# Performance work log

Measured on AMD Instinct MI355X. Metric: run time of the kernel, lower is better.

## Reference

```python
import jax, jax.numpy as jnp
from jax import lax
import numpy as np

NH = 4                      # num_heads in CrossScaleCom
KS = [3, 5, 7, 9]           # per-head depthwise kernel sizes
WS = 2                      # window_size in LocalFeatureGuided
GGM_K = 7                   # guide-token generator kernel size


def _dwconv(x, w, stride, pad):
    # depthwise conv: w has shape (C, 1, k, k), feature_group_count = C
    return lax.conv_general_dilated(
        x, w, (stride, stride), [(pad, pad), (pad, pad)],
        feature_group_count=x.shape[1],
        dimension_numbers=("NCHW", "OIHW", "NCHW"))


def _forward(x, dw_w0, dw_b0, dw_w1, dw_b1, dw_w2, dw_b2, dw_w3, dw_b3,
             csc_w, csc_b, bn_gamma, bn_beta, bn_mean, bn_var,
             ggm_w, ggm_b, qkv_w, qkv_b, proj_w, proj_b):
    B, C, H, W = x.shape
    cph = C // NH
    # ---- CrossScaleCom: per-head multi-scale depthwise convs ----
    xh = x.reshape(B, NH, cph, H, W)
    dws = [(dw_w0, dw_b0), (dw_w1, dw_b1), (dw_w2, dw_b2), (dw_w3, dw_b3)]
    heads = [_dwconv(xh[:, i], w, 1, KS[i] // 2) + b[None, :, None, None]
             for i, (w, b) in enumerate(dws)]
    y = jnp.stack(heads, 1)                      # (B, NH, cph, H, W)
    y = y.transpose(0, 2, 1, 3, 4).reshape(B, C, H, W)  # channel shuffle
    y = jnp.einsum("bchw,oc->bohw", y, csc_w) + csc_b[None, :, None, None]
    Co = y.shape[1]
    # ---- LocalFeatureGuided ----
    # ggm: BatchNorm (eval) -> GELU (exact) -> depthwise conv k=7 stride=WS
    inv = bn_gamma / jnp.sqrt(bn_var + 1e-5)
    g = (y - bn_mean[None, :, None, None]) * inv[None, :, None, None] \
        + bn_beta[None, :, None, None]
    g = jax.nn.gelu(g, approximate=False)
    g = _dwconv(g, ggm_w, WS, GGM_K // 2) + ggm_b[None, :, None, None]  # (B,Co,Ho,Wo)
    Ho, Wo = H // WS, W // WS
    L = Ho * Wo
    # unfold(kernel=WS, stride=WS) -> (B, Co, WS*WS, L), torch unfold ordering
    xu = y.reshape(B, Co, Ho, WS, Wo, WS).transpose(0, 1, 3, 5, 2, 4)
    xu = xu.reshape(B, Co, WS * WS, L)
    tokens = jnp.concatenate([g.reshape(B, Co, 1, L), xu], axis=2)  # (B,Co,5,L)
    # 1x1 conv over channel dim == einsum
    qkv = jnp.einsum("bcpl,oc->bopl", tokens, qkv_w) + qkv_b[None, :, None, None]
    q, k, v = jnp.split(qkv, 3, axis=1)          # each (B, Co, 5, L)
    # tiny 5x5 attention per (batch, channel), contracting over windows L
    attn = jnp.einsum("bcpl,bcql->bcpq", q, k) / (Co ** 0.5)
    attn = jax.nn.softmax(attn, axis=-1)
    out = jnp.einsum("bcpq,bcql->bcpl", attn, v)  # (B, Co, 5, L)
    out = out[:, :, 0, :].reshape(B, Co, Ho, Wo)  # guide-token output
    out = jnp.einsum("bchw,oc->bohw", out, proj_w) + proj_b[None, :, None, None]
    return out


def setup_inputs() -> dict:
    key = jax.random.key(0)
    ks = jax.random.split(key, 16)
    B, Cin, Cout, H, W = 8, 64, 128, 224, 224
    cph = Cin // NH
    s = 0.05
    d = {"x": jax.random.normal(ks[0], (B, Cin, H, W), jnp.float32)}
    for i, kk in enumerate(KS):
        d[f"dw_w{i}"] = jax.random.normal(ks[1 + i], (cph, 1, kk, kk), jnp.float32) * s
        d[f"dw_b{i}"] = jnp.zeros((cph,), jnp.float32)
    d["csc_w"] = jax.random.normal(ks[5], (Cout, Cin), jnp.float32) * s
    d["csc_b"] = jnp.zeros((Cout,), jnp.float32)
    d["bn_gamma"] = jnp.ones((Cout,), jnp.float32)
    d["bn_beta"] = jnp.zeros((Cout,), jnp.float32)
    d["bn_mean"] = jnp.zeros((Cout,), jnp.float32)
    d["bn_var"] = jnp.ones((Cout,), jnp.float32)
    d["ggm_w"] = jax.random.normal(ks[6], (Cout, 1, GGM_K, GGM_K), jnp.float32) * s
    d["ggm_b"] = jnp.zeros((Cout,), jnp.float32)
    d["qkv_w"] = jax.random.normal(ks[7], (3 * Cout, Cout), jnp.float32) * s
    d["qkv_b"] = jnp.zeros((3 * Cout,), jnp.float32)
    d["proj_w"] = jax.random.normal(ks[8], (Cout, Cout), jnp.float32) * s
    d["proj_b"] = jnp.zeros((Cout,), jnp.float32)
    return d


def reference(x, dw_w0, dw_b0, dw_w1, dw_b1, dw_w2, dw_b2, dw_w3, dw_b3,
              csc_w, csc_b, bn_gamma, bn_beta, bn_mean, bn_var,
              ggm_w, ggm_b, qkv_w, qkv_b, proj_w, proj_b):
    return _forward(x, dw_w0, dw_b0, dw_w1, dw_b1, dw_w2, dw_b2, dw_w3, dw_b3,
                    csc_w, csc_b, bn_gamma, bn_beta, bn_mean, bn_var,
                    ggm_w, ggm_b, qkv_w, qkv_b, proj_w, proj_b)
```

## Files before the change

kernel.cpp:

```cpp
#include <hip/hip_runtime.h>

#define BB 8
#define CIN 64
#define CO 128
#define Hdim 224
#define Wdim 224
#define HWt (224*224)
#define HO 112
#define WO 112
#define Lt (112*112)

typedef unsigned short u16;
typedef short bf16x8 __attribute__((ext_vector_type(8)));
typedef float f32x4  __attribute__((ext_vector_type(4)));
#define MFMA16(a,b,c) __builtin_amdgcn_mfma_f32_16x16x32_bf16((a),(b),(c),0,0,0)

__device__ inline u16 f2bf(float f) {
    union { float f; unsigned u; } v; v.f = f;
    unsigned r = (v.u + 0x7fffu + ((v.u >> 16) & 1u)) >> 16;
    return (u16)r;
}
__device__ inline float bf2f(u16 h) {
    union { unsigned u; float f; } v; v.u = ((unsigned)h) << 16; return v.f;
}
__device__ inline float uasf(unsigned u) {
    union { unsigned u; float f; } v; v.u = u; return v.f;
}

__device__ inline float gelu_fast(float x) {
    float z  = x * 0.7071067811865476f;
    float az = fabsf(z);
    float t  = __builtin_amdgcn_rcpf(fmaf(0.3275911f, az, 1.0f));
    float p  = fmaf(fmaf(fmaf(fmaf(1.061405429f, t, -1.453152027f), t,
                    1.421413741f), t, -0.284496736f), t, 0.254829592f);
    float e  = __expf(-z * z);
    float er = copysignf(1.0f - p * t * e, z);
    return 0.5f * x * (1.0f + er);
}

template<int HEAD>
__global__ __launch_bounds__(256) void dw_conv(
    const float* __restrict__ x, const float* __restrict__ w,
    const float* __restrict__ bias, u16* __restrict__ dwb)
{
    constexpr int K   = 3 + 2*HEAD;
    constexpr int PAD = HEAD + 1;
    constexpr int R   = 32 + 2*PAD;
    const int tile = blockIdx.x;
    const int c    = blockIdx.y;
    const int b    = blockIdx.z;
    const int th = (tile/7)*32, tw = (tile%7)*32;
    __shared__ float patch[R*40];
    const int tid = threadIdx.x;
    const float* xin = x + (size_t)(b*CIN + HEAD*16 + c)*HWt;
    for (int idx = tid; idx < R*40; idx += 256) {
        int r = idx / 40, cc = idx - r*40;
        int gy = th - PAD + r, gx = tw - 4 + cc;
        float v = 0.f;
        if (gy >= 0 && gy < Hdim && gx >= 0 && gx < Wdim) v = xin[gy*Wdim + gx];
        patch[idx] = v;
    }
    float wreg[K*K];
    const float* wp = w + c*K*K;
    #pragma unroll
    for (int i = 0; i < K*K; i++) wreg[i] = wp[i];
    const float bv = bias[c];
    __syncthreads();

    const int ty = tid >> 3, x0 = (tid & 7) * 4;
    float acc[4] = {bv, bv, bv, bv};
    #pragma unroll
    for (int ky = 0; ky < K; ky++) {
        float rr[12];
        *(float4*)&rr[0] = *(const float4*)&patch[(ty+ky)*40 + x0];
        *(float4*)&rr[4] = *(const float4*)&patch[(ty+ky)*40 + x0 + 4];
        *(float4*)&rr[8] = *(const float4*)&patch[(ty+ky)*40 + x0 + 8];
        #pragma unroll
        for (int kx = 0; kx < K; kx++) {
            const float wv = wreg[ky*K + kx];
            #pragma unroll
            for (int j = 0; j < 4; j++)
                acc[j] = fmaf(rr[j + kx + 4 - PAD], wv, acc[j]);
        }
    }
    const int s = c*4 + HEAD;
    u16 o4[4] = {f2bf(acc[0]), f2bf(acc[1]), f2bf(acc[2]), f2bf(acc[3])};
    *(uint2*)&dwb[(size_t)(b*CIN + s)*HWt + (th+ty)*Wdim + tw + x0] = *(uint2*)o4;
}

__global__ __launch_bounds__(256) void csc_mfma(
    const float* __restrict__ W, const float* __restrict__ bias,
    const u16* __restrict__ dwb, u16* __restrict__ y4)
{
    const int b  = blockIdx.z;
    const int p0 = blockIdx.x * 128;
    __shared__ u16 Abuf[128*72];
    __shared__ u16 Tbuf[32*132];
    const int tid = threadIdx.x;
    const int wv = tid >> 6, ln = tid & 63;
    const int mh = (wv >> 1)*64, nh = (wv & 1)*64;
    const int lm = ln & 15, kq = ln >> 4;
    for (int t = tid; t < 1024; t += 256) {
        int r = t >> 3, kk = (t & 7)*8;
        const float* src = &W[r*64 + kk];
        float4 f0 = *(const float4*)src, f1 = *(const float4*)(src+4);
        u16 tmp[8] = {f2bf(f0.x),f2bf(f0.y),f2bf(f0.z),f2bf(f0.w),
                      f2bf(f1.x),f2bf(f1.y),f2bf(f1.z),f2bf(f1.w)};
        *(uint4*)&Abuf[r*72 + kk] = *(uint4*)tmp;
    }
    const u16* Db = dwb + (size_t)b*CIN*HWt;
    f32x4 acc[4][4];
    #pragma unroll
    for (int i=0;i<4;i++)
        #pragma unroll
        for (int j=0;j<4;j++) acc[i][j] = (f32x4){0.f,0.f,0.f,0.f};

    for (int kc = 0; kc < 64; kc += 32) {
        __syncthreads();
        for (int t = tid; t < 512; t += 256) {
            int k = t >> 4, n0 = (t & 15)*8;
            *(uint4*)&Tbuf[k*132 + n0] = *(const uint4*)&Db[(size_t)(kc+k)*HWt + p0 + n0];
        }
        __syncthreads();
        bf16x8 af[4], bfr[4];
        #pragma unroll
        for (int tm=0;tm<4;tm++)
            af[tm] = *(bf16x8*)&Abuf[(mh + tm*16 + lm)*72 + kc + kq*8];
        #pragma unroll
        for (int tn=0;tn<4;tn++) {
            int n = nh + tn*16 + lm;
            #pragma unroll
            for (int j=0;j<8;j++) bfr[tn][j] = (short)Tbuf[(kq*8+j)*132 + n];
        }
        #pragma unroll
        for (int tm=0;tm<4;tm++)
            #pragma unroll
            for (int tn=0;tn<4;tn++)
                acc[tm][tn] = MFMA16(af[tm], bfr[tn], acc[tm][tn]);
    }
    #pragma unroll
    for (int tm=0;tm<4;tm++) {
        #pragma unroll
        for (int r=0;r<4;r++) {
            int o = mh + tm*16 + kq*4 + r;
            float bb = bias[o];
            #pragma unroll
            for (int tn=0;tn<4;tn++) {
                int p = p0 + nh + tn*16 + lm;
                int gy = p / 224, gx = p - gy*224;
                int w = (gy&1)*2 + (gx&1);
                y4[((size_t)(b*CO + o)*4 + w)*Lt + (gy>>1)*WO + (gx>>1)]
                    = f2bf(acc[tm][tn][r] + bb);
            }
        }
    }
}

__global__ __launch_bounds__(512) void ggm_kernel(const u16* __restrict__ y4,
    const float* __restrict__ gamma, const float* __restrict__ beta,
    const float* __restrict__ mean, const float* __restrict__ var,
    const float* __restrict__ gw, const float* __restrict__ gb,
    u16* __restrict__ gbf)
{
    const int ho0 = blockIdx.x * 16;
    const int c   = blockIdx.y;
    const int b   = blockIdx.z;
    __shared__ float patch[37*240];
    const int tid = threadIdx.x;

    const float inv = gamma[c] * rsqrtf(var[c] + 1e-5f);
    const float bsh = fmaf(-mean[c], inv, beta[c]);
    const u16* ybc = y4 + (size_t)(b*CO + c)*4*Lt;

    float wk[49];
    const float* wp = gw + c*49;
    #pragma unroll
    for (int i = 0; i < 49; i++) wk[i] = wp[i];
    const float bv = gb[c];

    for (int idx = tid; idx < 37*60; idx += 512) {
        int r = idx / 60, j = idx - r*60;
        int gy = 2*ho0 - 3 + r;
        float4 v = make_float4(0.f, 0.f, 0.f, 0.f);
        if (gy >= 0 && gy < Hdim && j >= 2 && j <= 57) {
            const u16* pe = ybc + (size_t)((gy&1)*2)*Lt + (gy>>1)*WO + (2*j - 4);
            unsigned e = *(const unsigned*)pe;
            unsigned o = *(const unsigned*)(pe + Lt);
            v.x = gelu_fast(fmaf(uasf(e << 16),         inv, bsh));
            v.y = gelu_fast(fmaf(uasf(o << 16),         inv, bsh));
            v.z = gelu_fast(fmaf(uasf(e & 0xffff0000u), inv, bsh));
            v.w = gelu_fast(fmaf(uasf(o & 0xffff0000u), inv, bsh));
        }
        *(float4*)&patch[idx*4] = v;
    }
    __syncthreads();

    if (tid < 448) {
        const int n = tid % 56;
        const int g = tid / 56;
        float acc[2][2] = {{bv, bv}, {bv, bv}};
        #pragma unroll
        for (int rr = 0; rr < 9; rr++) {
            const float* row = &patch[(4*g + rr)*240 + 4*n + 4];
            float f[12];
            *(float4*)&f[0] = *(const float4*)&row[0];
            *(float4*)&f[4] = *(const float4*)&row[4];
            *(float4*)&f[8] = *(const float4*)&row[8];
            #pragma unroll
            for (int i = 0; i < 2; i++) {
                const int ky = rr - 2*i;
                if (ky >= 0 && ky <= 6) {
                    #pragma unroll
                    for (int kx = 0; kx < 7; kx++) {
                        const float wv = wk[ky*7 + kx];
                        acc[i][0] = fmaf(f[kx + 1], wv, acc[i][0]);
                        acc[i][1] = fmaf(f[kx + 3], wv, acc[i][1]);
                    }
                }
            }
        }
        u16* gout = gbf + (size_t)(b*CO + c)*Lt;
        #pragma unroll
        for (int i = 0; i < 2; i++) {
            u16 o2[2] = {f2bf(acc[i][0]), f2bf(acc[i][1])};
            *(unsigned*)&gout[(ho0 + 2*g + i)*WO + 2*n] = *(unsigned*)o2;
        }
    }
}

__global__ __launch_bounds__(256) void G_mfma(
    const u16* __restrict__ gbf, const u16* __restrict__ y4,
    float* __restrict__ Gpart, float* __restrict__ Spart)
{
    const int b = blockIdx.z, p = blockIdx.y, split = blockIdx.x;
    const u16* Ab = gbf + (size_t)b*CO*Lt;
    const u16* Bb; int brs;
    if (p == 0) { Bb = Ab; brs = Lt; }
    else        { Bb = y4 + ((size_t)b*CO*4 + (p-1))*Lt; brs = 4*Lt; }
    __shared__ u16 Abuf[128*72];
    __shared__ u16 Bbuf[128*72];
    const int tid = threadIdx.x;
    const int wv = tid >> 6, ln = tid & 63;
    const int mh = (wv >> 1)*64, nh = (wv & 1)*64;
    const int lm = ln & 15, kq = ln >> 4;
    f32x4 acc[4][4];
    #pragma unroll
    for (int i=0;i<4;i++)
        #pragma unroll
        for (int j=0;j<4;j++) acc[i][j] = (f32x4){0.f,0.f,0.f,0.f};
    bf16x8 af_s;
    #pragma unroll
    for (int j=0;j<8;j++) af_s[j] = (lm == 0) ? (short)0x3F80 : (short)0;
    f32x4 acc_s[4];
    #pragma unroll
    for (int j=0;j<4;j++) acc_s[j] = (f32x4){0.f,0.f,0.f,0.f};
    const bool sWave = (mh == 0);

    for (int ci = split; ci < 196; ci += 16) {
        const int l0 = ci*64;
        __syncthreads();
        for (int t = tid; t < 1024; t += 256) {
            int r = t >> 3, kk = (t & 7)*8;
            *(uint4*)&Abuf[r*72 + kk] = *(const uint4*)&Ab[(size_t)r*Lt  + l0 + kk];
            *(uint4*)&Bbuf[r*72 + kk] = *(const uint4*)&Bb[(size_t)r*brs + l0 + kk];
        }
        __syncthreads();
        #pragma unroll
        for (int ks = 0; ks < 2; ks++) {
            bf16x8 af[4], bfr[4];
            #pragma unroll
            for (int tm=0;tm<4;tm++)
                af[tm]  = *(bf16x8*)&Abuf[(mh + tm*16 + lm)*72 + ks*32 + kq*8];
            #pragma unroll
            for (int tn=0;tn<4;tn++)
                bfr[tn] = *(bf16x8*)&Bbuf[(nh + tn*16 + lm)*72 + ks*32 + kq*8];
            #pragma unroll
            for (int tm=0;tm<4;tm++)
                #pragma unroll
                for (int tn=0;tn<4;tn++)
                    acc[tm][tn] = MFMA16(af[tm], bfr[tn], acc[tm][tn]);
            if (sWave) {
                #pragma unroll
                for (int tn=0;tn<4;tn++)
                    acc_s[tn] = MFMA16(af_s, bfr[tn], acc_s[tn]);
            }
        }
    }
    float* Go = Gpart + ((size_t)(split*40) + b*5 + p)*CO*CO;
    #pragma unroll
    for (int tm=0;tm<4;tm++)
        #pragma unroll
        for (int r=0;r<4;r++) {
            int mrow = mh + tm*16 + kq*4 + r;
            #pragma unroll
            for (int tn=0;tn<4;tn++)
                Go[mrow*CO + nh + tn*16 + lm] = acc[tm][tn][r];
        }
    if (sWave && kq == 0) {
        float* So = Spart + ((size_t)(split*40) + b*5 + p)*CO;
        #pragma unroll
        for (int tn=0;tn<4;tn++)
            So[nh + tn*16 + lm] = acc_s[tn][0];
    }
}

__global__ void G_reduce(const float* __restrict__ Gpart,
                         const float* __restrict__ Spart,
                         float* __restrict__ G, float* __restrict__ S)
{
    const int bp = blockIdx.x;
    const int i4 = (blockIdx.y*256 + threadIdx.x)*4;
    float4 s = make_float4(0.f, 0.f, 0.f, 0.f);
    #pragma unroll
    for (int sp = 0; sp < 16; sp++) {
        float4 v = *(const float4*)&Gpart[((size_t)(sp*40) + bp)*CO*CO + i4];
        s.x += v.x; s.y += v.y; s.z += v.z; s.w += v.w;
    }
    *(float4*)&G[(size_t)bp*CO*CO + i4] = s;
    if (blockIdx.y == 0 && threadIdx.x < CO) {
        float ss = 0.f;
        #pragma unroll
        for (int sp = 0; sp < 16; sp++)
            ss += Spart[((size_t)(sp*40) + bp)*CO + threadIdx.x];
        S[(size_t)bp*CO + threadIdx.x] = ss;
    }
}

__global__ __launch_bounds__(256) void fused_logits_kernel(
    const float* __restrict__ G, const float* __restrict__ S,
    const float* __restrict__ qkv_w, const float* __restrict__ qkv_b,
    float* __restrict__ lg)
{
    const int p = blockIdx.x, b = blockIdx.y;
    __shared__ float Wl[32*132];
    __shared__ float Al[32*132];
    __shared__ float KGl[128*128];
    const int tid = threadIdx.x;
    const int og = (tid >> 4) * 8;
    const int pg = (tid & 15) * 8;
    const float* Gp = G + (size_t)(b*5 + p)*CO*CO;
    float acc[8][8];
    #pragma unroll
    for (int i=0;i<8;i++)
        #pragma unroll
        for (int j=0;j<8;j++) acc[i][j]=0.f;

    for (int kc = 0; kc < 128; kc += 32) {
        __syncthreads();
        for (int t = tid; t < 4096; t += 256) {
            int kk = t & 31, o = t >> 5;
            Wl[kk*132 + o] = Gp[(size_t)o*CO + kc + kk];
            Al[kk*132 + o] = qkv_w[(size_t)(CO + o)*CO + kc + kk];
        }
        __syncthreads();
        #pragma unroll 4
        for (int kk = 0; kk < 32; kk++) {
            float wv[8], av[8];
            *(float4*)&wv[0] = *(const float4*)&Wl[kk*132+og];
            *(float4*)&wv[4] = *(const float4*)&Wl[kk*132+og+4];
            *(float4*)&av[0] = *(const float4*)&Al[kk*132+pg];
            *(float4*)&av[4] = *(const float4*)&Al[kk*132+pg+4];
            #pragma unroll
            for (int i=0;i<8;i++)
                #pragma unroll
                for (int j=0;j<8;j++)
                    acc[i][j] = fmaf(wv[i], av[j], acc[i][j]);
        }
    }
    #pragma unroll
    for (int i=0;i<8;i++) {
        #pragma unroll
        for (int j=0;j<8;j+=4)
            *(float4*)&KGl[(og+i)*128 + pg + j] = *(float4*)&acc[i][j];
    }
    __syncthreads();
    if (tid < 128) {
        const int c = tid;
        const float qb = qkv_b[c], kb = qkv_b[CO + c];
        const float* S0 = S + (size_t)b*5*CO;
        const float* Sp = S0 + p*CO;
        const float* qwrow = qkv_w + (size_t)c*CO;
        const float* kwrow = qkv_w + (size_t)(CO + c)*CO;
        float sq = qb * 12544.f, ks = 0.f, s = 0.f;
        for (int c2 = 0; c2 < CO; c2++) {
            sq = fmaf(qwrow[c2], S0[c2], sq);
            ks = fmaf(kwrow[c2], Sp[c2], ks);
            s  = fmaf(qwrow[c2], KGl[c2*128 + c], s);
        }
        lg[(size_t)(b*5 + p)*CO + c] = s + qb*ks + kb*sq;
    }
}

__global__ void softmax5_kernel(const float* __restrict__ lg, float* __restrict__ a)
{
    const int b = blockIdx.x, c = threadIdx.x;
    float v[5];
    #pragma unroll
    for (int p=0;p<5;p++) v[p] = lg[(size_t)(b*5 + p)*CO + c];
    const float scl = 0.08838834764831845f;
    float mx = v[0];
    #pragma unroll
    for (int p=1;p<5;p++) mx = fmaxf(mx, v[p]);
    float e[5], sum = 0.f;
    #pragma unroll
    for (int p=0;p<5;p++){ e[p] = __expf((v[p]-mx)*scl); sum += e[p]; }
    const float rs = 1.f/sum;
    #pragma unroll
    for (int p=0;p<5;p++) a[((size_t)b*CO + c)*5 + p] = e[p]*rs;
}

__global__ void F_kernel(const float* __restrict__ proj_w,
    const float* __restrict__ qkv_w, const float* __restrict__ a,
    u16* __restrict__ Fb)
{
    const int b = blockIdx.z, p = blockIdx.y;
    const int o  = blockIdx.x*2 + (threadIdx.x>>7);
    const int cp = threadIdx.x & 127;
    const float* vw = qkv_w + 2*CO*CO;
    float s = 0.f;
    for (int c=0;c<CO;c++)
        s = fmaf(proj_w[o*CO+c] * a[((size_t)b*CO+c)*5 + p], vw[c*CO+cp], s);
    Fb[(((size_t)(b*5+p))*CO + o)*CO + cp] = f2bf(s);
}

__global__ void bias_kernel(const float* __restrict__ proj_w,
    const float* __restrict__ proj_b, const float* __restrict__ qkv_b,
    float* __restrict__ biasout)
{
    const int o = threadIdx.x;
    const float* vb = qkv_b + 2*CO;
    float s = proj_b[o];
    for (int c=0;c<CO;c++) s = fmaf(proj_w[o*CO+c], vb[c], s);
    biasout[o] = s;
}

__global__ __launch_bounds__(256) void final_mfma(
    const u16* __restrict__ Fb, const u16* __restrict__ gbf,
    const u16* __restrict__ y4, const float* __restrict__ biasout,
    float* __restrict__ out)
{
    const int b = blockIdx.z;
    const int p0 = blockIdx.x * 128;
    __shared__ u16 Abuf[128*40];
    __shared__ u16 Tbuf[32*132];
    const int tid = threadIdx.x;
    const int wv = tid >> 6, ln = tid & 63;
    const int mh = (wv >> 1)*64, nh = (wv & 1)*64;
    const int lm = ln & 15, kq = ln >> 4;
    f32x4 acc[4][4];
    #pragma unroll
    for (int i=0;i<4;i++)
        #pragma unroll
        for (int j=0;j<4;j++) acc[i][j] = (f32x4){0.f,0.f,0.f,0.f};

    for (int ph = 0; ph < 5; ph++) {
        const u16* Fp = Fb + (size_t)(b*5 + ph)*CO*CO;
        const u16* Bb; int brs;
        if (ph == 0) { Bb = gbf + (size_t)b*CO*Lt; brs = Lt; }
        else         { Bb = y4 + ((size_t)b*CO*4 + (ph-1))*Lt; brs = 4*Lt; }
        for (int kc = 0; kc < CO; kc += 32) {
            __syncthreads();
            for (int t = tid; t < 512; t += 256) {
                int r = t >> 2, kk = (t & 3)*8;
                *(uint4*)&Abuf[r*40 + kk] = *(const uint4*)&Fp[r*CO + kc + kk];
            }
            for (int t = tid; t < 512; t += 256) {
                int k = t >> 4, n0 = (t & 15)*8;
                *(uint4*)&Tbuf[k*132 + n0] = *(const uint4*)&Bb[(size_t)(kc+k)*brs + p0 + n0];
            }
            __syncthreads();
            bf16x8 af[4], bfr[4];
            #pragma unroll
            for (int tm=0;tm<4;tm++)
                af[tm] = *(bf16x8*)&Abuf[(mh + tm*16 + lm)*40 + kq*8];
            #pragma unroll
            for (int tn=0;tn<4;tn++) {
                int n = nh + tn*16 + lm;
                #pragma unroll
                for (int j=0;j<8;j++) bfr[tn][j] = (short)Tbuf[(kq*8+j)*132 + n];
            }
            #pragma unroll
            for (int tm=0;tm<4;tm++)
                #pragma unroll
                for (int tn=0;tn<4;tn++)
                    acc[tm][tn] = MFMA16(af[tm], bfr[tn], acc[tm][tn]);
        }
    }
    float* Ob = out + (size_t)b*CO*Lt;
    #pragma unroll
    for (int tm=0;tm<4;tm++) {
        #pragma unroll
        for (int r=0;r<4;r++) {
            int o = mh + tm*16 + kq*4 + r;
            float bb = biasout[o];
            #pragma unroll
            for (int tn=0;tn<4;tn++)
                Ob[(size_t)o*Lt + p0 + nh + tn*16 + lm] = acc[tm][tn][r] + bb;
        }
    }
}

extern "C" void kernel_launch(void* const* d_in, const int* in_sizes, int n_in,
                              void* d_out, int out_size, void* d_ws, size_t ws_size,
                              hipStream_t stream) {
    const float* x      = (const float*)d_in[0];
    const float* dw_w0  = (const float*)d_in[1];
    const float* dw_b0  = (const float*)d_in[2];
    const float* dw_w1  = (const float*)d_in[3];
    const float* dw_b1  = (const float*)d_in[4];
    const float* dw_w2  = (const float*)d_in[5];
    const float* dw_b2  = (const float*)d_in[6];
    const float* dw_w3  = (const float*)d_in[7];
    const float* dw_b3  = (const float*)d_in[8];
    const float* csc_w  = (const float*)d_in[9];
    const float* csc_b  = (const float*)d_in[10];
    const float* bn_g   = (const float*)d_in[11];
    const float* bn_b   = (const float*)d_in[12];
    const float* bn_m   = (const float*)d_in[13];
    const float* bn_v   = (const float*)d_in[14];
    const float* ggm_w  = (const float*)d_in[15];
    const float* ggm_b  = (const float*)d_in[16];
    const float* qkv_w  = (const float*)d_in[17];
    const float* qkv_b  = (const float*)d_in[18];
    const float* proj_w = (const float*)d_in[19];
    const float* proj_b = (const float*)d_in[20];
    float* out = (float*)d_out;

    char* ws = (char*)d_ws;
    u16*   y4  = (u16*)(ws);
    u16*   dwb = (u16*)(ws + 102760448);
    u16*   gbf = (u16*)(ws + 154140672);
    float* G   = (float*)(ws + 179830784);
    float* lgb = (float*)(ws + 182452224);
    u16*   Fb  = (u16*)  (ws + 182472704);
    float* S   = (float*)(ws + 183783424);
    float* aw  = (float*)(ws + 183803904);
    float* bo  = (float*)(ws + 183824384);
    float* Gpart = (float*)(ws + 102760448);
    float* Spart = (float*)(ws + 144703488);

    dw_conv<0><<<dim3(49, 16, 8), 256, 0, stream>>>(x, dw_w0, dw_b0, dwb);
    dw_conv<1><<<dim3(49, 16, 8), 256, 0, stream>>>(x, dw_w1, dw_b1, dwb);
    dw_conv<2><<<dim3(49, 16, 8), 256, 0, stream>>>(x, dw_w2, dw_b2, dwb);
    dw_conv<3><<<dim3(49, 16, 8), 256, 0, stream>>>(x, dw_w3, dw_b3, dwb);

    csc_mfma<<<dim3(392, 1, 8), 256, 0, stream>>>(csc_w, csc_b, dwb, y4);

    ggm_kernel<<<dim3(7, 128, 8), 512, 0, stream>>>(
        y4, bn_g, bn_b, bn_m, bn_v, ggm_w, ggm_b, gbf);

    G_mfma<<<dim3(16, 5, 8), 256, 0, stream>>>(gbf, y4, Gpart, Spart);
    G_reduce<<<dim3(40, 16), 256, 0, stream>>>(Gpart, Spart, G, S);

    fused_logits_kernel<<<dim3(5, 8), 256, 0, stream>>>(G, S, qkv_w, qkv_b, lgb);

    softmax5_kernel<<<dim3(8), 128, 0, stream>>>(lgb, aw);

    F_kernel<<<dim3(64, 5, 8), 256, 0, stream>>>(proj_w, qkv_w, aw, Fb);
    bias_kernel<<<dim3(1), 128, 0, stream>>>(proj_w, proj_b, qkv_b, bo);

    final_mfma<<<dim3(98, 1, 8), 256, 0, stream>>>(Fb, gbf, y4, bo, out);
}
```

Before: 617.7 us.

## Tile csc GEMM in 2D spatially for paired stores; widen G split when workspace allows

The csc_mfma kernel now tiles pixels as 4 rows by 32 columns and permutes the columns inside shared memory. Each lane then holds two horizontally adjacent pixels of the same unfold window and writes them as one 32-bit store into y4, where before it issued scattered 16-bit stores. Separately, G_mfma raises its split-K count from 16 to 32 when the workspace is large enough, giving more blocks for the 40 (batch, token) GEMMs at the cost of more partial sums for G_reduce to add. Shared-memory staging becomes scalar scattered 16-bit writes, which may add bank conflicts.

```diff
diff --git a/kernel.cpp b/kernel.cpp
--- a/kernel.cpp
+++ b/kernel.cpp
@@ -92,8 +92,9 @@
     const float* __restrict__ W, const float* __restrict__ bias,
     const u16* __restrict__ dwb, u16* __restrict__ y4)
 {
-    const int b  = blockIdx.z;
-    const int p0 = blockIdx.x * 128;
+    const int b   = blockIdx.z;
+    const int gy0 = (blockIdx.x / 7) * 4;
+    const int gx0 = (blockIdx.x % 7) * 32;
     __shared__ u16 Abuf[128*72];
     __shared__ u16 Tbuf[32*132];
     const int tid = threadIdx.x;
@@ -118,8 +119,20 @@
     for (int kc = 0; kc < 64; kc += 32) {
         __syncthreads();
         for (int t = tid; t < 512; t += 256) {
-            int k = t >> 4, n0 = (t & 15)*8;
-            *(uint4*)&Tbuf[k*132 + n0] = *(const uint4*)&Db[(size_t)(kc+k)*HWt + p0 + n0];
+            int k = t >> 4, s = t & 15;
+            int ry = s >> 2, seg = s & 3;
+            uint4 v = *(const uint4*)&Db[(size_t)(kc+k)*HWt
+                                         + (gy0+ry)*224 + gx0 + seg*8];
+            unsigned uu[4] = {v.x, v.y, v.z, v.w};
+            #pragma unroll
+            for (int u = 0; u < 8; u++) {
+                int gxo = seg*8 + u;
+                int lmd = ((gxo >> 2) << 1) | (gxo & 1);
+                int tnd = ((gxo >> 1) & 1) | ((ry & 1) << 1);
+                int nhd = (ry >> 1) << 6;
+                u16 val = (u16)((uu[u >> 1] >> ((u & 1)*16)) & 0xffff);
+                Tbuf[k*132 + nhd + tnd*16 + lmd] = val;
+            }
         }
         __syncthreads();
         bf16x8 af[4], bfr[4];
@@ -138,19 +151,22 @@
             for (int tn=0;tn<4;tn++)
                 acc[tm][tn] = MFMA16(af[tm], bfr[tn], acc[tm][tn]);
     }
+    const int gyh = (gy0 >> 1) + (nh >> 6);
+    const int gxh = (gx0 >> 1) + 2*(lm >> 1);
     #pragma unroll
     for (int tm=0;tm<4;tm++) {
         #pragma unroll
         for (int r=0;r<4;r++) {
             int o = mh + tm*16 + kq*4 + r;
             float bb = bias[o];
-            #pragma unroll
-            for (int tn=0;tn<4;tn++) {
-                int p = p0 + nh + tn*16 + lm;
-                int gy = p / 224, gx = p - gy*224;
-                int w = (gy&1)*2 + (gx&1);
-                y4[((size_t)(b*CO + o)*4 + w)*Lt + (gy>>1)*WO + (gx>>1)]
-                    = f2bf(acc[tm][tn][r] + bb);
+            size_t obase = (size_t)(b*CO + o)*4*Lt;
+            #pragma unroll
+            for (int pr=0;pr<2;pr++) {
+                int w = (pr << 1) | (lm & 1);
+                u16 p2[2] = {f2bf(acc[tm][2*pr][r] + bb),
+                             f2bf(acc[tm][2*pr+1][r] + bb)};
+                *(unsigned*)&y4[obase + (size_t)w*Lt + gyh*WO + gxh]
+                    = *(unsigned*)p2;
             }
         }
     }
@@ -230,7 +246,7 @@
 
 __global__ __launch_bounds__(256) void G_mfma(
     const u16* __restrict__ gbf, const u16* __restrict__ y4,
-    float* __restrict__ Gpart, float* __restrict__ Spart)
+    float* __restrict__ Gpart, float* __restrict__ Spart, int nsplit)
 {
     const int b = blockIdx.z, p = blockIdx.y, split = blockIdx.x;
     const u16* Ab = gbf + (size_t)b*CO*Lt;
@@ -256,7 +272,7 @@
     for (int j=0;j<4;j++) acc_s[j] = (f32x4){0.f,0.f,0.f,0.f};
     const bool sWave = (mh == 0);
 
-    for (int ci = split; ci < 196; ci += 16) {
+    for (int ci = split; ci < 196; ci += nsplit) {
         const int l0 = ci*64;
         __syncthreads();
         for (int t = tid; t < 1024; t += 256) {
@@ -306,21 +322,20 @@
 
 __global__ void G_reduce(const float* __restrict__ Gpart,
                          const float* __restrict__ Spart,
-                         float* __restrict__ G, float* __restrict__ S)
+                         float* __restrict__ G, float* __restrict__ S,
+                         int nsplit)
 {
     const int bp = blockIdx.x;
     const int i4 = (blockIdx.y*256 + threadIdx.x)*4;
     float4 s = make_float4(0.f, 0.f, 0.f, 0.f);
-    #pragma unroll
-    for (int sp = 0; sp < 16; sp++) {
+    for (int sp = 0; sp < nsplit; sp++) {
         float4 v = *(const float4*)&Gpart[((size_t)(sp*40) + bp)*CO*CO + i4];
         s.x += v.x; s.y += v.y; s.z += v.z; s.w += v.w;
     }
     *(float4*)&G[(size_t)bp*CO*CO + i4] = s;
     if (blockIdx.y == 0 && threadIdx.x < CO) {
         float ss = 0.f;
-        #pragma unroll
-        for (int sp = 0; sp < 16; sp++)
+        for (int sp = 0; sp < nsplit; sp++)
             ss += Spart[((size_t)(sp*40) + bp)*CO + threadIdx.x];
         S[(size_t)bp*CO + threadIdx.x] = ss;
     }
@@ -536,8 +551,11 @@
     float* S   = (float*)(ws + 183783424);
     float* aw  = (float*)(ws + 183803904);
     float* bo  = (float*)(ws + 183824384);
-    float* Gpart = (float*)(ws + 102760448);
-    float* Spart = (float*)(ws + 144703488);
+
+    const bool big = ws_size >= (size_t)268366336;
+    const int nsplit = big ? 32 : 16;
+    float* Gpart = big ? (float*)(ws + 183824896) : (float*)(ws + 102760448);
+    float* Spart = Gpart + (size_t)nsplit*40*CO*CO;
 
     dw_conv<0><<<dim3(49, 16, 8), 256, 0, stream>>>(x, dw_w0, dw_b0, dwb);
     dw_conv<1><<<dim3(49, 16, 8), 256, 0, stream>>>(x, dw_w1, dw_b1, dwb);
@@ -549,8 +567,8 @@
     ggm_kernel<<<dim3(7, 128, 8), 512, 0, stream>>>(
         y4, bn_g, bn_b, bn_m, bn_v, ggm_w, ggm_b, gbf);
 
-    G_mfma<<<dim3(16, 5, 8), 256, 0, stream>>>(gbf, y4, Gpart, Spart);
-    G_reduce<<<dim3(40, 16), 256, 0, stream>>>(Gpart, Spart, G, S);
+    G_mfma<<<dim3(nsplit, 5, 8), 256, 0, stream>>>(gbf, y4, Gpart, Spart, nsplit);
+    G_reduce<<<dim3(40, 16), 256, 0, stream>>>(Gpart, Spart, G, S, nsplit);
 
     fused_logits_kernel<<<dim3(5, 8), 256, 0, stream>>>(G, S, qkv_w, qkv_b, lgb);
 
```

Measured after the change: 656.0 us. +6.2%, slower.
